# Kernel tuning notes

Measured on AMD Instinct MI355X. Metric: run time of the kernel, lower is better.

## Reference

```python
import jax, jax.numpy as jnp
import numpy as np

NUM_SEGMENTS = 64  # number of bags
L, D, F = 1024, 256, 32  # D = L/4, F = D/8, K = 1
EPS = 1e-12  # torch F.normalize eps


def setup_inputs() -> dict:
    key = jax.random.key(0)
    ks = jax.random.split(key, 10)
    N = 262144
    x = jax.random.normal(ks[0], (N, L), dtype=jnp.float32)
    idxs = jnp.sort(jax.random.randint(ks[1], (N,), 0, NUM_SEGMENTS)).astype(jnp.int64)
    sc = lambda fan_in: 1.0 / np.sqrt(fan_in)
    W1 = jax.random.uniform(ks[2], (L, D), jnp.float32, -sc(L), sc(L))
    b1 = jax.random.uniform(ks[3], (D,), jnp.float32, -sc(L), sc(L))
    Wa1 = jax.random.uniform(ks[4], (D, F), jnp.float32, -sc(D), sc(D))
    ba1 = jax.random.uniform(ks[5], (F,), jnp.float32, -sc(D), sc(D))
    Wa2 = jax.random.uniform(ks[6], (F, 1), jnp.float32, -sc(F), sc(F))
    ba2 = jax.random.uniform(ks[7], (1,), jnp.float32, -sc(F), sc(F))
    Wp = jax.random.uniform(ks[8], (D, F), jnp.float32, -sc(D), sc(D))
    bp = jax.random.uniform(ks[9], (F,), jnp.float32, -sc(D), sc(D))
    return {"x": x, "idxs": idxs, "W1": W1, "b1": b1, "Wa1": Wa1, "ba1": ba1,
            "Wa2": Wa2, "ba2": ba2, "Wp": Wp, "bp": bp}


def reference(x, idxs, W1, b1, Wa1, ba1, Wa2, ba2, Wp, bp):
    seg = idxs.astype(jnp.int32)
    # feature extractor (Dropout is identity in eval): H [N, D]
    H = x @ W1 + b1
    # attention logits: tanh MLP -> [N]
    logits = (jnp.tanh(H @ Wa1 + ba1) @ Wa2 + ba2)[:, 0]
    # segment softmax over instances within each bag
    m = jax.ops.segment_max(logits, seg, num_segments=NUM_SEGMENTS)
    e = jnp.exp(logits - m[seg])
    s = jax.ops.segment_sum(e, seg, num_segments=NUM_SEGMENTS)
    w = e / s[seg]  # [N]
    # attention-weighted bag embeddings: M [B, D]
    M = jax.ops.segment_sum(w[:, None] * H, seg, num_segments=NUM_SEGMENTS)
    # projector + L2 normalize (torch F.normalize: x / max(||x||, eps))
    proj = M @ Wp + bp
    norm = jnp.linalg.norm(proj, axis=1, keepdims=True)
    proj = proj / jnp.maximum(norm, EPS)
    return (M, proj)
```

## Files before the change

### kernel.cpp

```cpp
#include <hip/hip_runtime.h>
#include <stdint.h>

#define LDIM 1024
#define DDIM 256
#define FDIM 32
#define NSEG 64
#define BM 64
#define BK 64

typedef __attribute__((ext_vector_type(4))) float f32x4;
typedef __attribute__((ext_vector_type(8))) short short8;
typedef __attribute__((ext_vector_type(4))) unsigned int u32x4;

__device__ __forceinline__ unsigned int pk2bf(float a, float b) {
  union { float f; unsigned int u; } x, y; x.f = a; y.f = b;
  unsigned int ua = x.u + 0x7FFFu + ((x.u >> 16) & 1u);
  unsigned int ub = y.u + 0x7FFFu + ((y.u >> 16) & 1u);
  return (ua >> 16) | (ub & 0xFFFF0000u);
}

__device__ __forceinline__ unsigned short f2bf(float f) {
  union { float f; unsigned int u; } v; v.f = f;
  unsigned int r = v.u + 0x7FFFu + ((v.u >> 16) & 1u);
  return (unsigned short)(r >> 16);
}

__global__ void prep_w1t(const float* __restrict__ W1, const float* __restrict__ Wa1,
                         unsigned short* __restrict__ w1t) {
  __shared__ float rowf[DDIM];
  const int k = blockIdx.x;
  const int t = threadIdx.x;
  float v = W1[(size_t)k * DDIM + t];
  rowf[t] = v;
  w1t[(size_t)t * LDIM + k] = f2bf(v);
  __syncthreads();
  if (t < FDIM) {
    float a = 0.f;
    for (int c = 0; c < DDIM; ++c) a += rowf[c] * Wa1[c * FDIM + t];
    w1t[(size_t)(DDIM + t) * LDIM + k] = f2bf(a);
  }
}

__global__ void prep_misc(const float* __restrict__ b1, const float* __restrict__ Wa1,
                          const float* __restrict__ ba1, float* __restrict__ bz,
                          float* __restrict__ acc_eh, float* __restrict__ accE) {
  const int b = blockIdx.x, t = threadIdx.x;
  acc_eh[b * DDIM + t] = 0.f;
  if (t == 0) accE[b] = 0.f;
  if (b == 0 && t < FDIM) {
    float a = ba1[t];
    for (int c = 0; c < DDIM; ++c) a += b1[c] * Wa1[c * FDIM + t];
    bz[t] = a;
  }
}

__global__ __launch_bounds__(256, 3) void fused_main(
    const float* __restrict__ x, const int* __restrict__ idxs,
    const unsigned short* __restrict__ w1t, const float* __restrict__ bz,
    const float* __restrict__ Wa2, const float* __restrict__ ba2,
    float* __restrict__ acc_eh, float* __restrict__ accE)
{
  __shared__ __align__(16) unsigned short xlds[BM][72];
  __shared__ __align__(16) unsigned char blds[288 * 128];
  __shared__ float logit_s[BM];
  __shared__ float e_s[BM];
  __shared__ int seg_s[BM];

  const int tid = threadIdx.x;
  const int lane = tid & 63;
  const int wid = tid >> 6;
  const int wr = wid >> 1;
  const int wc = wid & 1;
  const int g = lane >> 4;
  const int cl = lane & 15;
  const int row0 = blockIdx.x * BM;

  if (tid < BM) seg_s[tid] = idxs[row0 + tid];

  f32x4 acc[2][9];
  const f32x4 zero4 = {0.f, 0.f, 0.f, 0.f};
  #pragma unroll
  for (int m = 0; m < 2; ++m)
    #pragma unroll
    for (int n = 0; n < 9; ++n) acc[m][n] = zero4;

  const int arow = tid >> 2;
  const int aq = tid & 3;
  const char* w1tb = (const char*)w1t;

  f32x4 r0, r1, r2, r3;
  {
    const float* gx = x + (size_t)(row0 + arow) * LDIM + aq * 16;
    r0 = *(const f32x4*)(gx);
    r1 = *(const f32x4*)(gx + 4);
    r2 = *(const f32x4*)(gx + 8);
    r3 = *(const f32x4*)(gx + 12);
  }

  #pragma unroll 1
  for (int kt = 0; kt < 16; ++kt) {
    __syncthreads();
    #pragma unroll
    for (int j = 0; j < 9; ++j) {
      int byteoff = j * 4096 + tid * 16;
      int brow = byteoff >> 7;
      int bcolb = byteoff & 127;
      int srcb = brow * 2048 + kt * 128 + (bcolb ^ ((brow & 7) << 4));
      __builtin_amdgcn_global_load_lds(
          (const __attribute__((address_space(1))) unsigned int*)(w1tb + srcb),
          (__attribute__((address_space(3))) unsigned int*)(blds + j * 4096 + wid * 1024),
          16, 0, 0);
    }
    u32x4 p0, p1;
    p0[0] = pk2bf(r0[0], r0[1]); p0[1] = pk2bf(r0[2], r0[3]);
    p0[2] = pk2bf(r1[0], r1[1]); p0[3] = pk2bf(r1[2], r1[3]);
    p1[0] = pk2bf(r2[0], r2[1]); p1[1] = pk2bf(r2[2], r2[3]);
    p1[2] = pk2bf(r3[0], r3[1]); p1[3] = pk2bf(r3[2], r3[3]);
    *(u32x4*)&xlds[arow][aq * 16] = p0;
    *(u32x4*)&xlds[arow][aq * 16 + 8] = p1;
    __syncthreads();
    if (kt < 15) {
      const float* gx = x + (size_t)(row0 + arow) * LDIM + (kt + 1) * BK + aq * 16;
      r0 = *(const f32x4*)(gx);
      r1 = *(const f32x4*)(gx + 4);
      r2 = *(const f32x4*)(gx + 8);
      r3 = *(const f32x4*)(gx + 12);
    }
    #pragma unroll
    for (int kk = 0; kk < 2; ++kk) {
      short8 af0 = *(const short8*)((const char*)xlds + (wr * 32 + cl) * 144 + kk * 64 + g * 16);
      short8 af1 = *(const short8*)((const char*)xlds + (wr * 32 + 16 + cl) * 144 + kk * 64 + g * 16);
      #pragma unroll
      for (int n = 0; n < 9; ++n) {
        int brr = wc * 144 + n * 16 + cl;
        short8 bf = *(const short8*)(blds + brr * 128 + ((kk * 64 + g * 16) ^ ((brr & 7) << 4)));
        acc[0][n] = __builtin_amdgcn_mfma_f32_16x16x32_bf16(af0, bf, acc[0][n], 0, 0, 0);
        acc[1][n] = __builtin_amdgcn_mfma_f32_16x16x32_bf16(af1, bf, acc[1][n], 0, 0, 0);
      }
    }
  }

  if (wc == 1) {
    const float w2a = Wa2[cl], w2b = Wa2[16 + cl];
    const float bza = bz[cl], bzb = bz[16 + cl];
    #pragma unroll
    for (int m = 0; m < 2; ++m) {
      float p[4];
      #pragma unroll
      for (int q = 0; q < 4; ++q) {
        float ea = exp2f((acc[m][7][q] + bza) * 2.8853900817779268f);
        float eb = exp2f((acc[m][8][q] + bzb) * 2.8853900817779268f);
        p[q] = (1.f - 2.f / (ea + 1.f)) * w2a + (1.f - 2.f / (eb + 1.f)) * w2b;
      }
      #pragma unroll
      for (int mask = 1; mask <= 8; mask <<= 1)
        #pragma unroll
        for (int q = 0; q < 4; ++q) p[q] += __shfl_xor(p[q], mask);
      if (cl == 0) {
        #pragma unroll
        for (int q = 0; q < 4; ++q)
          logit_s[wr * 32 + m * 16 + g * 4 + q] = p[q];
      }
    }
  }
  __syncthreads();
  if (tid < BM) e_s[tid] = expf(logit_s[tid] + ba2[0]);
  __syncthreads();

  const int smin = seg_s[0];
  const int smax = seg_s[BM - 1];
  float ev[8]; int sv[8];
  #pragma unroll
  for (int m = 0; m < 2; ++m)
    #pragma unroll
    for (int q = 0; q < 4; ++q) {
      int rl = wr * 32 + m * 16 + g * 4 + q;
      ev[m * 4 + q] = e_s[rl];
      sv[m * 4 + q] = seg_s[rl];
    }
  for (int s = smin; s <= smax; ++s) {
    float wv[8];
    #pragma unroll
    for (int i = 0; i < 8; ++i) wv[i] = (sv[i] == s) ? ev[i] : 0.f;
    #pragma unroll
    for (int n = 0; n < 9; ++n) {
      if (n < 7 || wc == 0) {
        float cs = 0.f;
        #pragma unroll
        for (int m = 0; m < 2; ++m)
          #pragma unroll
          for (int q = 0; q < 4; ++q)
            cs += wv[m * 4 + q] * acc[m][n][q];
        cs += __shfl_xor(cs, 16);
        cs += __shfl_xor(cs, 32);
        if (lane < 16) atomicAdd(&acc_eh[s * DDIM + wc * 144 + n * 16 + cl], cs);
      }
    }
    if (wid == 0) {
      float v = (seg_s[lane] == s) ? e_s[lane] : 0.f;
      #pragma unroll
      for (int mask = 1; mask <= 32; mask <<= 1) v += __shfl_xor(v, mask);
      if (lane == 0) atomicAdd(&accE[s], v);
    }
  }
}

__global__ void finalize_k(const float* __restrict__ acc_eh, const float* __restrict__ accE,
                           const float* __restrict__ b1, const float* __restrict__ Wp,
                           const float* __restrict__ bp, float* __restrict__ out) {
  __shared__ float Ml[DDIM];
  const int s = blockIdx.x, t = threadIdx.x;
  const float E = accE[s];
  float m = 0.f;
  if (E > 0.f) m = acc_eh[s * DDIM + t] / E + b1[t];
  out[s * DDIM + t] = m;
  Ml[t] = m;
  __syncthreads();
  if (t < FDIM) {
    float p = bp[t];
    for (int c = 0; c < DDIM; ++c) p += Ml[c] * Wp[c * FDIM + t];
    float n2 = p * p;
    #pragma unroll
    for (int mask = 1; mask <= 16; mask <<= 1) n2 += __shfl_xor(n2, mask);
    out[NSEG * DDIM + s * FDIM + t] = p / fmaxf(sqrtf(n2), 1e-12f);
  }
}

extern "C" void kernel_launch(void* const* d_in, const int* in_sizes, int n_in,
                              void* d_out, int out_size, void* d_ws, size_t ws_size,
                              hipStream_t stream) {
  const float* x   = (const float*)d_in[0];
  const int*   idxs= (const int*)d_in[1];
  const float* W1  = (const float*)d_in[2];
  const float* b1  = (const float*)d_in[3];
  const float* Wa1 = (const float*)d_in[4];
  const float* ba1 = (const float*)d_in[5];
  const float* Wa2 = (const float*)d_in[6];
  const float* ba2 = (const float*)d_in[7];
  const float* Wp  = (const float*)d_in[8];
  const float* bp  = (const float*)d_in[9];
  float* out = (float*)d_out;

  char* ws = (char*)d_ws;
  unsigned short* w1t = (unsigned short*)ws;
  float* bz     = (float*)(ws + 655360);
  float* acc_eh = (float*)(ws + 655488);
  float* accE   = (float*)(ws + 721024);

  const int n = in_sizes[1];
  prep_w1t<<<LDIM, DDIM, 0, stream>>>(W1, Wa1, w1t);
  prep_misc<<<NSEG, DDIM, 0, stream>>>(b1, Wa1, ba1, bz, acc_eh, accE);
  fused_main<<<n / BM, 256, 0, stream>>>(x, idxs, w1t, bz, Wa2, ba2, acc_eh, accE);
  finalize_k<<<NSEG, DDIM, 0, stream>>>(acc_eh, accE, b1, Wp, bp, out);
}
```

Baseline: 291.2 us.

## Load x fragments directly into MFMA registers, bypassing LDS staging

Each wave now loads its own x rows straight from global memory in the MFMA operand layout and converts them to bf16 in registers, removing the shared-memory x tile, its stores and its reads. The barriers are replaced with a raw s_barrier and an explicit vmcnt wait so the next tile's x prefetch can stay in flight while the W1 LDS loads complete. Because both column-wave pairs read the same rows, each x element is fetched from global memory twice, and the hand-written waitcnt depends on how the compiler orders the loads.

Result: slower. 394.3 us (+35.4%).

```diff
diff --git a/kernel.cpp b/kernel.cpp
--- a/kernel.cpp
+++ b/kernel.cpp
@@ -23,6 +23,13 @@
   union { float f; unsigned int u; } v; v.f = f;
   unsigned int r = v.u + 0x7FFFu + ((v.u >> 16) & 1u);
   return (unsigned short)(r >> 16);
+}
+
+__device__ __forceinline__ short8 pack8(f32x4 a, f32x4 b) {
+  union { u32x4 u; short8 s; } r;
+  r.u[0] = pk2bf(a[0], a[1]); r.u[1] = pk2bf(a[2], a[3]);
+  r.u[2] = pk2bf(b[0], b[1]); r.u[3] = pk2bf(b[2], b[3]);
+  return r.s;
 }
 
 __global__ void prep_w1t(const float* __restrict__ W1, const float* __restrict__ Wa1,
@@ -60,7 +67,6 @@
     const float* __restrict__ Wa2, const float* __restrict__ ba2,
     float* __restrict__ acc_eh, float* __restrict__ accE)
 {
-  __shared__ __align__(16) unsigned short xlds[BM][72];
   __shared__ __align__(16) unsigned char blds[288 * 128];
   __shared__ float logit_s[BM];
   __shared__ float e_s[BM];
@@ -84,22 +90,22 @@
     #pragma unroll
     for (int n = 0; n < 9; ++n) acc[m][n] = zero4;
 
-  const int arow = tid >> 2;
-  const int aq = tid & 3;
   const char* w1tb = (const char*)w1t;
 
-  f32x4 r0, r1, r2, r3;
+  const float* a0 = x + (size_t)(row0 + wr * 32 + cl) * LDIM + g * 8;
+  const float* a1 = a0 + (size_t)16 * LDIM;
+
+  f32x4 s00, s01, s02, s03, s10, s11, s12, s13;
   {
-    const float* gx = x + (size_t)(row0 + arow) * LDIM + aq * 16;
-    r0 = *(const f32x4*)(gx);
-    r1 = *(const f32x4*)(gx + 4);
-    r2 = *(const f32x4*)(gx + 8);
-    r3 = *(const f32x4*)(gx + 12);
+    s00 = *(const f32x4*)(a0);      s01 = *(const f32x4*)(a0 + 4);
+    s02 = *(const f32x4*)(a0 + 32); s03 = *(const f32x4*)(a0 + 36);
+    s10 = *(const f32x4*)(a1);      s11 = *(const f32x4*)(a1 + 4);
+    s12 = *(const f32x4*)(a1 + 32); s13 = *(const f32x4*)(a1 + 36);
   }
 
   #pragma unroll 1
   for (int kt = 0; kt < 16; ++kt) {
-    __syncthreads();
+    __builtin_amdgcn_s_barrier();
     #pragma unroll
     for (int j = 0; j < 9; ++j) {
       int byteoff = j * 4096 + tid * 16;
@@ -111,31 +117,28 @@
           (__attribute__((address_space(3))) unsigned int*)(blds + j * 4096 + wid * 1024),
           16, 0, 0);
     }
-    u32x4 p0, p1;
-    p0[0] = pk2bf(r0[0], r0[1]); p0[1] = pk2bf(r0[2], r0[3]);
-    p0[2] = pk2bf(r1[0], r1[1]); p0[3] = pk2bf(r1[2], r1[3]);
-    p1[0] = pk2bf(r2[0], r2[1]); p1[1] = pk2bf(r2[2], r2[3]);
-    p1[2] = pk2bf(r3[0], r3[1]); p1[3] = pk2bf(r3[2], r3[3]);
-    *(u32x4*)&xlds[arow][aq * 16] = p0;
-    *(u32x4*)&xlds[arow][aq * 16 + 8] = p1;
-    __syncthreads();
-    if (kt < 15) {
-      const float* gx = x + (size_t)(row0 + arow) * LDIM + (kt + 1) * BK + aq * 16;
-      r0 = *(const f32x4*)(gx);
-      r1 = *(const f32x4*)(gx + 4);
-      r2 = *(const f32x4*)(gx + 8);
-      r3 = *(const f32x4*)(gx + 12);
-    }
+    short8 af00 = pack8(s00, s01);
+    short8 af01 = pack8(s02, s03);
+    short8 af10 = pack8(s10, s11);
+    short8 af11 = pack8(s12, s13);
+    {
+      int ktn = (kt < 15) ? (kt + 1) : 15;
+      const float* p0 = a0 + ktn * 64;
+      const float* p1 = a1 + ktn * 64;
+      s00 = *(const f32x4*)(p0);      s01 = *(const f32x4*)(p0 + 4);
+      s02 = *(const f32x4*)(p0 + 32); s03 = *(const f32x4*)(p0 + 36);
+      s10 = *(const f32x4*)(p1);      s11 = *(const f32x4*)(p1 + 4);
+      s12 = *(const f32x4*)(p1 + 32); s13 = *(const f32x4*)(p1 + 36);
+    }
+    asm volatile("s_waitcnt vmcnt(8)\n\ts_barrier" ::: "memory");
     #pragma unroll
     for (int kk = 0; kk < 2; ++kk) {
-      short8 af0 = *(const short8*)((const char*)xlds + (wr * 32 + cl) * 144 + kk * 64 + g * 16);
-      short8 af1 = *(const short8*)((const char*)xlds + (wr * 32 + 16 + cl) * 144 + kk * 64 + g * 16);
       #pragma unroll
       for (int n = 0; n < 9; ++n) {
         int brr = wc * 144 + n * 16 + cl;
         short8 bf = *(const short8*)(blds + brr * 128 + ((kk * 64 + g * 16) ^ ((brr & 7) << 4)));
-        acc[0][n] = __builtin_amdgcn_mfma_f32_16x16x32_bf16(af0, bf, acc[0][n], 0, 0, 0);
-        acc[1][n] = __builtin_amdgcn_mfma_f32_16x16x32_bf16(af1, bf, acc[1][n], 0, 0, 0);
+        acc[0][n] = __builtin_amdgcn_mfma_f32_16x16x32_bf16(kk ? af01 : af00, bf, acc[0][n], 0, 0, 0);
+        acc[1][n] = __builtin_amdgcn_mfma_f32_16x16x32_bf16(kk ? af11 : af10, bf, acc[1][n], 0, 0, 0);
       }
     }
   }
```
